# Optimization experiments

Measured on AMD Instinct MI355X. Metric: run time of the kernel, lower is better.

The kernel has to match this reference:

```python
import jax, jax.numpy as jnp
import numpy as np

B, H, W, C = 2, 384, 384, 64
WIN = 8
HEADS = 2
HD = C // HEADS
SCALE = HD ** -0.5
HID = 256  # mlp_ratio * dim
N = WIN * WIN


def _rel_index():
    # Swin-style relative position index, computed once with numpy (static).
    coords = np.stack(np.meshgrid(np.arange(WIN), np.arange(WIN), indexing='ij'))  # 2,w,w
    cf = coords.reshape(2, -1)
    rel = cf[:, :, None] - cf[:, None, :]            # 2,N,N
    rel = rel.transpose(1, 2, 0).astype(np.int64)    # N,N,2
    rel[..., 0] += WIN - 1
    rel[..., 1] += WIN - 1
    rel[..., 0] *= 2 * WIN - 1
    return jnp.asarray(rel.sum(-1))                  # N,N

REL_IDX = _rel_index()


def _ln(x, g, b):
    m = x.mean(-1, keepdims=True)
    v = ((x - m) ** 2).mean(-1, keepdims=True)
    return (x - m) * jax.lax.rsqrt(v + 1e-5) * g + b


def setup_inputs() -> dict:
    key = jax.random.key(0)
    ks = jax.random.split(key, 10)
    def n(k, shape, s=0.02):
        return jax.random.normal(k, shape, jnp.float32) * s
    return {
        'x': jax.random.normal(ks[0], (B, H * W, C), jnp.float32),
        'norm1_g': jnp.ones((C,), jnp.float32), 'norm1_b': jnp.zeros((C,), jnp.float32),
        'wq': n(ks[1], (C, C)), 'bq': jnp.zeros((C,), jnp.float32),
        'wkv': n(ks[2], (C, 2 * C)), 'bkv': jnp.zeros((2 * C,), jnp.float32),
        'rel_bias': n(ks[3], ((2 * WIN - 1) ** 2, HEADS)),
        'wproj': n(ks[4], (C, C)), 'bproj': jnp.zeros((C,), jnp.float32),
        'norm2_g': jnp.ones((C,), jnp.float32), 'norm2_b': jnp.zeros((C,), jnp.float32),
        'w1': n(ks[5], (C, HID)), 'b1': jnp.zeros((HID,), jnp.float32),
        'dwk': n(ks[6], (HID, 1, 3, 3)), 'dwb': jnp.zeros((HID,), jnp.float32),
        'w2': n(ks[7], (HID, C)), 'b2': jnp.zeros((C,), jnp.float32),
    }


def _forward(x, norm1_g, norm1_b, wq, bq, wkv, bkv, rel_bias, wproj, bproj,
             norm2_g, norm2_b, w1, b1, dwk, dwb, w2, b2):
    # --- windowed self-attention (shift_size=0, no mask) ---
    xs = _ln(x, norm1_g, norm1_b).reshape(B, H, W, C)
    win = xs.reshape(B, H // WIN, WIN, W // WIN, WIN, C)
    win = win.transpose(0, 1, 3, 2, 4, 5).reshape(-1, N, C)     # (B*nW, N, C)
    q = (win @ wq + bq).reshape(-1, N, HEADS, HD).transpose(0, 2, 1, 3)
    kv = (win @ wkv + bkv).reshape(-1, N, 2, HEADS, HD)
    k = kv[:, :, 0].transpose(0, 2, 1, 3)
    v = kv[:, :, 1].transpose(0, 2, 1, 3)
    bias = rel_bias[REL_IDX].transpose(2, 0, 1)                 # (nH, N, N)
    attn = jnp.einsum('bhnd,bhmd->bhnm', q * SCALE, k) + bias[None]
    attn = jax.nn.softmax(attn, axis=-1)
    o = jnp.einsum('bhnm,bhmd->bhnd', attn, v)
    o = o.transpose(0, 2, 1, 3).reshape(-1, N, C) @ wproj + bproj
    # window reverse
    o = o.reshape(B, H // WIN, W // WIN, WIN, WIN, C)
    o = o.transpose(0, 1, 3, 2, 4, 5).reshape(B, H * W, C)
    x = x + o
    # --- LeFF: linear -> gelu -> depthwise 3x3 -> gelu -> linear ---
    y = _ln(x, norm2_g, norm2_b)
    h = jax.nn.gelu(y @ w1 + b1, approximate=False)
    hi = h.reshape(B, H, W, HID).transpose(0, 3, 1, 2)          # NCHW
    hi = jax.lax.conv_general_dilated(
        hi, dwk, window_strides=(1, 1), padding='SAME',
        feature_group_count=HID,
        dimension_numbers=('NCHW', 'OIHW', 'NCHW')) + dwb[None, :, None, None]
    h = jax.nn.gelu(hi, approximate=False).transpose(0, 2, 3, 1).reshape(B, H * W, HID)
    return x + (h @ w2 + b2)


def reference(x, norm1_g, norm1_b, wq, bq, wkv, bkv, rel_bias, wproj, bproj,
              norm2_g, norm2_b, w1, b1, dwk, dwb, w2, b2):
    return _forward(x, norm1_g, norm1_b, wq, bq, wkv, bkv, rel_bias, wproj, bproj,
                    norm2_g, norm2_b, w1, b1, dwk, dwb, w2, b2)
```

## Files before the change

### kernel.cpp

```cpp
#include <hip/hip_runtime.h>
#include <math.h>

typedef unsigned short u16;
typedef unsigned int u32;
typedef __attribute__((ext_vector_type(8))) unsigned short us8;
typedef __attribute__((ext_vector_type(8))) __bf16 bf16x8;
typedef __attribute__((ext_vector_type(4))) float f32x4;

#define MFMA16(a, b, c) __builtin_amdgcn_mfma_f32_16x16x32_bf16((a), (b), (c), 0, 0, 0)

static __device__ __forceinline__ float bf2f(u16 u) {
  union { u32 i; float f; } v; v.i = ((u32)u) << 16; return v.f;
}
static __device__ __forceinline__ u16 f2bf(float f) {
  __bf16 h = (__bf16)f;
  return __builtin_bit_cast(u16, h);
}
static __device__ __forceinline__ u32 pk2bf(float lo, float hi) {
  return ((u32)f2bf(hi) << 16) | (u32)f2bf(lo);
}
static __device__ __forceinline__ float lo16(u32 v) {
  union { u32 i; float f; } u; u.i = v << 16; return u.f;
}
static __device__ __forceinline__ float hi16(u32 v) {
  union { u32 i; float f; } u; u.i = v & 0xFFFF0000u; return u.f;
}
static __device__ __forceinline__ bf16x8 ldfrag(const u16* p) {
  us8 v = *reinterpret_cast<const us8*>(p);
  return __builtin_bit_cast(bf16x8, v);
}
static __device__ __forceinline__ float gelu_s(float x) {
  return x * __builtin_amdgcn_rcpf(1.0f + __builtin_amdgcn_exp2f(-2.45564427f * x));
}

#define NTOK 147456
#define NWX 48

__global__ __launch_bounds__(256) void k_prep(
    const float* __restrict__ wq, const float* __restrict__ wkv,
    const float* __restrict__ wproj, const float* __restrict__ w1,
    const float* __restrict__ w2, const float* __restrict__ relb,
    u16* __restrict__ wqkvT, u16* __restrict__ wpT,
    u16* __restrict__ w1T, u16* __restrict__ w2T, float* __restrict__ biasx)
{
  const int idx = blockIdx.x * 256 + threadIdx.x;
  const int NT = 64 * 256;
  for (int i = idx; i < 12288; i += NT) {
    int o = i >> 6, c = i & 63;
    wqkvT[i] = f2bf(o < 64 ? wq[c * 64 + o] : wkv[c * 128 + (o - 64)]);
  }
  for (int i = idx; i < 4096; i += NT) {
    int o = i >> 6, c = i & 63;
    wpT[i] = f2bf(wproj[c * 64 + o]);
  }
  for (int i = idx; i < 16384; i += NT) {
    int o = i >> 6, c = i & 63;
    w1T[i] = f2bf(w1[c * 256 + o]);
  }
  for (int i = idx; i < 16384; i += NT) {
    int o = i >> 8, c2 = i & 255;
    w2T[i] = f2bf(w2[c2 * 64 + o]);
  }
  for (int i = idx; i < 8192; i += NT) {
    int h = i >> 12, r = i & 4095, ii = r >> 6, j = r & 63;
    int dy = (ii >> 3) - (j >> 3) + 7, dx = (ii & 7) - (j & 7) + 7;
    biasx[i] = relb[(dy * 15 + dx) * 2 + h];
  }
}

static __device__ __forceinline__ void softmax_rows(
    const f32x4* sc, const float* biasrow_base, int i0, int lg, int lr,
    u16* Pd)
{
#pragma unroll
  for (int r = 0; r < 4; ++r) {
    const int i = i0 + lg * 4 + r;
    const float* brow = biasrow_base + i * 64;
    float pv[4];
    float mx = -1e30f;
#pragma unroll
    for (int jt = 0; jt < 4; ++jt) {
      pv[jt] = fmaf(sc[jt][r], 0.17677669529663687f, brow[jt * 16 + lr]);
      mx = fmaxf(mx, pv[jt]);
    }
#pragma unroll
    for (int off = 1; off < 16; off <<= 1) mx = fmaxf(mx, __shfl_xor(mx, off));
    float sum = 0.f;
#pragma unroll
    for (int jt = 0; jt < 4; ++jt) { pv[jt] = __expf(pv[jt] - mx); sum += pv[jt]; }
#pragma unroll
    for (int off = 1; off < 16; off <<= 1) sum += __shfl_xor(sum, off);
    const float inv = __builtin_amdgcn_rcpf(sum);
#pragma unroll
    for (int jt = 0; jt < 4; ++jt)
      Pd[i * 72 + jt * 16 + lr] = f2bf(pv[jt] * inv);
  }
}

__global__ __launch_bounds__(256, 4) void k_attn(
    const float* __restrict__ x,
    const float* __restrict__ n1g, const float* __restrict__ n1b,
    const u16* __restrict__ wqkvT, const float* __restrict__ bq,
    const float* __restrict__ bkv, const float* __restrict__ biasx,
    const u16* __restrict__ wpT, const float* __restrict__ bproj,
    float2* __restrict__ mrs, float* __restrict__ x1)
{
  __shared__ u16 xs[64 * 72];
  __shared__ u16 qsm[64 * 72];
  __shared__ u16 ksm[64 * 72];
  __shared__ u16 vT[64 * 72];

  const int tid = threadIdx.x;
  const int wv = tid >> 6;
  const int ln = tid & 63;
  const int lg = ln >> 4, lr = ln & 15;

  const int blk = blockIdx.x;
  const int b = blk / 2304;
  const int rem = blk - b * 2304;
  const int wy = rem / NWX, wx = rem - wy * NWX;

  {
    const int t = tid >> 2, g = tid & 3;
    const int gy = wy * 8 + (t >> 3), gx = wx * 8 + (t & 7);
    const long rowbase = ((long)b * NTOK + gy * 384 + gx) * 64;
    float loc[16];
    float s0 = 0.f, s1 = 0.f;
#pragma unroll
    for (int k = 0; k < 16; k += 4) {
      float4 v4 = *reinterpret_cast<const float4*>(x + rowbase + g * 16 + k);
      loc[k] = v4.x; loc[k + 1] = v4.y; loc[k + 2] = v4.z; loc[k + 3] = v4.w;
    }
#pragma unroll
    for (int k = 0; k < 16; ++k) { s0 += loc[k]; s1 += loc[k] * loc[k]; }
    s0 += __shfl_xor(s0, 1); s0 += __shfl_xor(s0, 2);
    s1 += __shfl_xor(s1, 1); s1 += __shfl_xor(s1, 2);
    const float m = s0 * 0.015625f;
    const float var = s1 * 0.015625f - m * m;
    const float rs = rsqrtf(var + 1e-5f);
#pragma unroll
    for (int k = 0; k < 16; ++k) {
      int c = g * 16 + k;
      xs[t * 72 + c] = f2bf((loc[k] - m) * rs * n1g[c] + n1b[c]);
    }
  }
  __syncthreads();

#pragma unroll
  for (int qq = 0; qq < 3; ++qq) {
    const int grp = 3 * wv + qq;
    const int n0 = grp * 16;
    const int oc = n0 + lr;
    const float bias = (grp < 4) ? bq[oc] : bkv[oc - 64];
    bf16x8 b0 = ldfrag(&wqkvT[oc * 64 + lg * 8]);
    bf16x8 b1 = ldfrag(&wqkvT[oc * 64 + 32 + lg * 8]);
#pragma unroll
    for (int ii = 0; ii < 4; ++ii) {
      const int i0 = ii * 16;
      f32x4 acc = { bias, bias, bias, bias };
      acc = MFMA16(ldfrag(&xs[(i0 + lr) * 72 + lg * 8]), b0, acc);
      acc = MFMA16(ldfrag(&xs[(i0 + lr) * 72 + 32 + lg * 8]), b1, acc);
      const int tok0 = i0 + lg * 4;
      if (grp < 4) {
#pragma unroll
        for (int r = 0; r < 4; ++r) qsm[(tok0 + r) * 72 + oc] = f2bf(acc[r]);
      } else if (grp < 8) {
#pragma unroll
        for (int r = 0; r < 4; ++r) ksm[(tok0 + r) * 72 + (oc - 64)] = f2bf(acc[r]);
      } else {
        u32* dst = reinterpret_cast<u32*>(&vT[(oc - 128) * 72 + tok0]);
        dst[0] = pk2bf(acc[0], acc[1]);
        dst[1] = pk2bf(acc[2], acc[3]);
      }
    }
  }
  __syncthreads();

  const int i0 = wv * 16;
  f32x4 oacc[2][2];
  {
    bf16x8 aq0 = ldfrag(&qsm[(i0 + lr) * 72 + lg * 8]);
    bf16x8 aq1 = ldfrag(&qsm[(i0 + lr) * 72 + 32 + lg * 8]);
    f32x4 sc0[4], sc1[4];
#pragma unroll
    for (int jt = 0; jt < 4; ++jt) {
      f32x4 z = {};
      bf16x8 bk0 = ldfrag(&ksm[(jt * 16 + lr) * 72 + lg * 8]);
      bf16x8 bk1 = ldfrag(&ksm[(jt * 16 + lr) * 72 + 32 + lg * 8]);
      sc0[jt] = MFMA16(aq0, bk0, z);
      sc1[jt] = MFMA16(aq1, bk1, z);
    }
    softmax_rows(sc0, biasx, i0, lg, lr, xs);
    softmax_rows(sc1, biasx + 4096, i0, lg, lr, qsm);

#pragma unroll
    for (int q = 0; q < 2; ++q) {
      f32x4 a0 = {}, a1 = {};
#pragma unroll
      for (int ks = 0; ks < 64; ks += 32) {
        a0 = MFMA16(ldfrag(&xs[(i0 + lr) * 72 + ks + lg * 8]),
                    ldfrag(&vT[(q * 16 + lr) * 72 + ks + lg * 8]), a0);
        a1 = MFMA16(ldfrag(&qsm[(i0 + lr) * 72 + ks + lg * 8]),
                    ldfrag(&vT[(32 + q * 16 + lr) * 72 + ks + lg * 8]), a1);
      }
      oacc[0][q] = a0;
      oacc[1][q] = a1;
    }
  }
  __syncthreads();

#pragma unroll
  for (int h = 0; h < 2; ++h)
#pragma unroll
    for (int q = 0; q < 2; ++q) {
      const int ch = h * 32 + q * 16 + lr;
#pragma unroll
      for (int r = 0; r < 4; ++r)
        ksm[(i0 + lg * 4 + r) * 72 + ch] = f2bf(oacc[h][q][r]);
    }

  {
    float s[4] = {}, sq[4] = {};
#pragma unroll
    for (int q = 0; q < 4; ++q) {
      const int o0 = q * 16;
      const int oc = o0 + lr;
      const float bp = bproj[oc];
      f32x4 acc = { bp, bp, bp, bp };
#pragma unroll
      for (int ks = 0; ks < 64; ks += 32) {
        bf16x8 ao = ldfrag(&ksm[(i0 + lr) * 72 + ks + lg * 8]);
        bf16x8 bw = ldfrag(&wpT[(o0 + lr) * 64 + ks + lg * 8]);
        acc = MFMA16(ao, bw, acc);
      }
#pragma unroll
      for (int r = 0; r < 4; ++r) {
        const int tok = i0 + lg * 4 + r;
        const int gy = wy * 8 + (tok >> 3), gx = wx * 8 + (tok & 7);
        const long idx = ((long)b * NTOK + gy * 384 + gx) * 64 + oc;
        const float v = x[idx] + acc[r];
        x1[idx] = v;
        s[r] += v; sq[r] += v * v;
      }
    }
#pragma unroll
    for (int r = 0; r < 4; ++r) {
      float ss = s[r], qq = sq[r];
#pragma unroll
      for (int off = 1; off < 16; off <<= 1) {
        ss += __shfl_xor(ss, off);
        qq += __shfl_xor(qq, off);
      }
      if (lr == 0) {
        const float m = ss * 0.015625f;
        const float var = qq * 0.015625f - m * m;
        const int tok = i0 + lg * 4 + r;
        const int gy = wy * 8 + (tok >> 3), gx = wx * 8 + (tok & 7);
        mrs[(long)b * NTOK + gy * 384 + gx] = make_float2(m, rsqrtf(var + 1e-5f));
      }
    }
  }
}

__global__ __launch_bounds__(512, 8) void k_mlp(
    const float* __restrict__ x1, const float2* __restrict__ mrs,
    const float* __restrict__ n2g, const float* __restrict__ n2b,
    const u16* __restrict__ w1T, const float* __restrict__ pb1,
    const float* __restrict__ dwk, const float* __restrict__ dwb,
    const u16* __restrict__ w2T, const float* __restrict__ pb2,
    float* __restrict__ out)
{
  __shared__ u16 xln[112 * 72];
  __shared__ u16 htbT[64 * 102];
  __shared__ u16 g2[64 * 72];
  __shared__ float flag[112];

  const int tid = threadIdx.x;
  const int wave = tid >> 6, ln = tid & 63;
  const int lg = ln >> 4, lr = ln & 15;
  const int blk = blockIdx.x;
  const int b = blk / 2304;
  const int rem = blk - b * 2304;
  const int ty0 = (rem / NWX) * 8, tx0 = (rem - (rem / NWX) * NWX) * 8;

  if (tid < 112) {
    float f = 0.f;
    if (tid < 100) {
      const int py = ty0 + tid / 10 - 1, px = tx0 + tid % 10 - 1;
      if (py >= 0 && py < 384 && px >= 0 && px < 384) f = 1.f;
    }
    flag[tid] = f;
  }

  {
    const float gg = n2g[ln], bb = n2b[ln];
#pragma unroll
    for (int j = 0; j < 14; ++j) {
      const int p = j * 8 + wave;
      u16 o = 0;
      if (p < 100) {
        const int py = ty0 + p / 10 - 1, px = tx0 + p % 10 - 1;
        if (py >= 0 && py < 384 && px >= 0 && px < 384) {
          const long tok = (long)b * NTOK + py * 384 + px;
          const float2 mr = mrs[tok];
          const float v = x1[tok * 64 + ln];
          o = f2bf((v - mr.x) * mr.y * gg + bb);
        }
      }
      xln[p * 72 + ln] = o;
    }
  }
  __syncthreads();

  const int n0f = (wave & 3) * 16;
  const int i0b = (wave >> 2) * 16;
  const int ocf = n0f + lr;
  const int o0  = (wave >> 1) * 16;
  const int i0q = ((wave * 2) & 3) * 16;
  const int oc2 = o0 + lr;
  const float fc2_b = pb2[oc2];
  f32x4 facc[2] = { { fc2_b, fc2_b, fc2_b, fc2_b }, { fc2_b, fc2_b, fc2_b, fc2_b } };

#pragma unroll 1
  for (int ch = 0; ch < 4; ++ch) {
    {
      const u16* wbase = &w1T[(ch * 64 + ocf) * 64 + lg * 8];
      bf16x8 wb0 = ldfrag(wbase);
      bf16x8 wb1 = ldfrag(wbase + 32);
      const float bias1 = pb1[ch * 64 + ocf];
#pragma unroll
      for (int k = 0; k < 4; ++k) {
        const int i0 = i0b + k * 32;
        if (i0 < 112) {
          f32x4 acc = { bias1, bias1, bias1, bias1 };
          acc = MFMA16(ldfrag(&xln[(i0 + lr) * 72 + lg * 8]), wb0, acc);
          acc = MFMA16(ldfrag(&xln[(i0 + lr) * 72 + 32 + lg * 8]), wb1, acc);
          const int p0 = i0 + lg * 4;
          if (p0 < 100) {
            float g0 = gelu_s(acc[0]) * flag[p0 + 0];
            float g1 = gelu_s(acc[1]) * flag[p0 + 1];
            float g2v = gelu_s(acc[2]) * flag[p0 + 2];
            float g3 = gelu_s(acc[3]) * flag[p0 + 3];
            u32* dst = reinterpret_cast<u32*>(&htbT[ocf * 102 + p0]);
            dst[0] = pk2bf(g0, g1);
            dst[1] = pk2bf(g2v, g3);
          }
        }
      }
    }
    __syncthreads();

    {
      const int gch = ch * 64 + ln;
      float wk[9];
      const float db = dwb[gch];
#pragma unroll
      for (int q = 0; q < 9; ++q) wk[q] = dwk[gch * 9 + q];
      const u16* rowbase = &htbT[ln * 102];
      const u32* r0 = reinterpret_cast<const u32*>(rowbase + (wave + 0) * 10);
      const u32* r1 = reinterpret_cast<const u32*>(rowbase + (wave + 1) * 10);
      const u32* r2 = reinterpret_cast<const u32*>(rowbase + (wave + 2) * 10);
      u32 v;
      float a0,b0,c0,d0, a1,b1,c1,d1, a2,b2,c2,d2;
      v = r0[0]; a0 = lo16(v); b0 = hi16(v);
      v = r0[1]; c0 = lo16(v); d0 = hi16(v);
      v = r1[0]; a1 = lo16(v); b1 = hi16(v);
      v = r1[1]; c1 = lo16(v); d1 = hi16(v);
      v = r2[0]; a2 = lo16(v); b2 = hi16(v);
      v = r2[1]; c2 = lo16(v); d2 = hi16(v);
#pragma unroll
      for (int s = 0; s < 4; ++s) {
        float e0 = db + a0 * wk[0] + b0 * wk[1] + c0 * wk[2]
                      + a1 * wk[3] + b1 * wk[4] + c1 * wk[5]
                      + a2 * wk[6] + b2 * wk[7] + c2 * wk[8];
        float e1 = db + b0 * wk[0] + c0 * wk[1] + d0 * wk[2]
                      + b1 * wk[3] + c1 * wk[4] + d1 * wk[5]
                      + b2 * wk[6] + c2 * wk[7] + d2 * wk[8];
        g2[(wave * 8 + 2 * s) * 72 + ln]     = f2bf(gelu_s(e0));
        g2[(wave * 8 + 2 * s + 1) * 72 + ln] = f2bf(gelu_s(e1));
        if (s < 3) {
          v = r0[s + 2]; a0 = c0; b0 = d0; c0 = lo16(v); d0 = hi16(v);
          v = r1[s + 2]; a1 = c1; b1 = d1; c1 = lo16(v); d1 = hi16(v);
          v = r2[s + 2]; a2 = c2; b2 = d2; c2 = lo16(v); d2 = hi16(v);
        }
      }
    }
    __syncthreads();

    {
      const u16* wbase2 = &w2T[oc2 * 256 + ch * 64 + lg * 8];
      bf16x8 bw0 = ldfrag(wbase2);
      bf16x8 bw1 = ldfrag(wbase2 + 32);
#pragma unroll
      for (int q = 0; q < 2; ++q) {
        const int i0 = i0q + q * 16;
        bf16x8 ag0 = ldfrag(&g2[(i0 + lr) * 72 + lg * 8]);
        bf16x8 ag1 = ldfrag(&g2[(i0 + lr) * 72 + 32 + lg * 8]);
        facc[q] = MFMA16(ag0, bw0, facc[q]);
        facc[q] = MFMA16(ag1, bw1, facc[q]);
      }
    }
  }

#pragma unroll
  for (int q = 0; q < 2; ++q) {
    const int i0 = i0q + q * 16;
#pragma unroll
    for (int r = 0; r < 4; ++r) {
      const int token = i0 + lg * 4 + r;
      const int gy = ty0 + (token >> 3), gx = tx0 + (token & 7);
      const long idx = ((long)b * NTOK + gy * 384 + gx) * 64 + oc2;
      out[idx] = x1[idx] + facc[q][r];
    }
  }
}

extern "C" void kernel_launch(void* const* d_in, const int* in_sizes, int n_in,
                              void* d_out, int out_size, void* d_ws, size_t ws_size,
                              hipStream_t stream) {
  const float* x     = (const float*)d_in[0];
  const float* n1g   = (const float*)d_in[1];
  const float* n1b   = (const float*)d_in[2];
  const float* wq    = (const float*)d_in[3];
  const float* bq    = (const float*)d_in[4];
  const float* wkv   = (const float*)d_in[5];
  const float* bkv   = (const float*)d_in[6];
  const float* relb  = (const float*)d_in[7];
  const float* wproj = (const float*)d_in[8];
  const float* bproj = (const float*)d_in[9];
  const float* n2g   = (const float*)d_in[10];
  const float* n2b   = (const float*)d_in[11];
  const float* w1    = (const float*)d_in[12];
  const float* b1    = (const float*)d_in[13];
  const float* dwk   = (const float*)d_in[14];
  const float* dwb   = (const float*)d_in[15];
  const float* w2    = (const float*)d_in[16];
  const float* b2    = (const float*)d_in[17];

  char* ws = (char*)d_ws;
  u16*    wqkvT = (u16*)ws;
  u16*    wpT   = (u16*)(ws + 24576);
  u16*    w1T   = (u16*)(ws + 32768);
  u16*    w2T   = (u16*)(ws + 65536);
  float*  biasx = (float*)(ws + 98304);
  float2* mrs   = (float2*)(ws + 131072);
  float*  x1    = (float*)(ws + 2490368);
  float*  outp  = (float*)d_out;

  k_prep<<<64, 256, 0, stream>>>(wq, wkv, wproj, w1, w2, relb, wqkvT, wpT, w1T, w2T, biasx);
  k_attn<<<4608, 256, 0, stream>>>(x, n1g, n1b, wqkvT, bq, bkv, biasx, wpT, bproj, mrs, x1);
  k_mlp<<<4608, 512, 0, stream>>>(x1, mrs, n2g, n2b, w1T, b1, dwk, dwb, w2T, b2, outp);
}
```

Baseline: 221.8 us.

## Store residual and LayerNorm2 output as bf16 intermediates from attention kernel

```diff
diff --git a/kernel.cpp b/kernel.cpp
--- a/kernel.cpp
+++ b/kernel.cpp
@@ -103,7 +103,8 @@
     const u16* __restrict__ wqkvT, const float* __restrict__ bq,
     const float* __restrict__ bkv, const float* __restrict__ biasx,
     const u16* __restrict__ wpT, const float* __restrict__ bproj,
-    float2* __restrict__ mrs, float* __restrict__ x1)
+    const float* __restrict__ n2g, const float* __restrict__ n2b,
+    u16* __restrict__ x1b, u16* __restrict__ xn)
 {
   __shared__ u16 xs[64 * 72];
   __shared__ u16 qsm[64 * 72];
@@ -220,29 +221,36 @@
     }
 
   {
+    const int tok0 = i0 + lg * 4;
+    const int gy0 = wy * 8 + (tok0 >> 3), gx0 = wx * 8 + (tok0 & 7);
+    const long xbase = ((long)b * NTOK + gy0 * 384 + gx0) * 64;
+
+    float vst[4][4];
     float s[4] = {}, sq[4] = {};
 #pragma unroll
     for (int q = 0; q < 4; ++q) {
-      const int o0 = q * 16;
-      const int oc = o0 + lr;
+      const int oc = q * 16 + lr;
       const float bp = bproj[oc];
       f32x4 acc = { bp, bp, bp, bp };
 #pragma unroll
       for (int ks = 0; ks < 64; ks += 32) {
         bf16x8 ao = ldfrag(&ksm[(i0 + lr) * 72 + ks + lg * 8]);
-        bf16x8 bw = ldfrag(&wpT[(o0 + lr) * 64 + ks + lg * 8]);
+        bf16x8 bw = ldfrag(&wpT[oc * 64 + ks + lg * 8]);
         acc = MFMA16(ao, bw, acc);
       }
+      long idx = xbase + oc;
 #pragma unroll
       for (int r = 0; r < 4; ++r) {
-        const int tok = i0 + lg * 4 + r;
-        const int gy = wy * 8 + (tok >> 3), gx = wx * 8 + (tok & 7);
-        const long idx = ((long)b * NTOK + gy * 384 + gx) * 64 + oc;
         const float v = x[idx] + acc[r];
-        x1[idx] = v;
+        x1b[idx] = f2bf(v);
+        vst[q][r] = v;
         s[r] += v; sq[r] += v * v;
-      }
-    }
+        idx += 64;
+      }
+    }
+    float ng[4], nb[4];
+#pragma unroll
+    for (int q = 0; q < 4; ++q) { ng[q] = n2g[q * 16 + lr]; nb[q] = n2b[q * 16 + lr]; }
 #pragma unroll
     for (int r = 0; r < 4; ++r) {
       float ss = s[r], qq = sq[r];
@@ -251,20 +259,18 @@
         ss += __shfl_xor(ss, off);
         qq += __shfl_xor(qq, off);
       }
-      if (lr == 0) {
-        const float m = ss * 0.015625f;
-        const float var = qq * 0.015625f - m * m;
-        const int tok = i0 + lg * 4 + r;
-        const int gy = wy * 8 + (tok >> 3), gx = wx * 8 + (tok & 7);
-        mrs[(long)b * NTOK + gy * 384 + gx] = make_float2(m, rsqrtf(var + 1e-5f));
-      }
+      const float m = ss * 0.015625f;
+      const float rs = rsqrtf(qq * 0.015625f - m * m + 1e-5f);
+      const long idxn = xbase + r * 64 + lr;
+#pragma unroll
+      for (int q = 0; q < 4; ++q)
+        xn[idxn + q * 16] = f2bf((vst[q][r] - m) * rs * ng[q] + nb[q]);
     }
   }
 }
 
 __global__ __launch_bounds__(512, 8) void k_mlp(
-    const float* __restrict__ x1, const float2* __restrict__ mrs,
-    const float* __restrict__ n2g, const float* __restrict__ n2b,
+    const u16* __restrict__ x1b, const u16* __restrict__ xn,
     const u16* __restrict__ w1T, const float* __restrict__ pb1,
     const float* __restrict__ dwk, const float* __restrict__ dwb,
     const u16* __restrict__ w2T, const float* __restrict__ pb2,
@@ -293,21 +299,21 @@
   }
 
   {
-    const float gg = n2g[ln], bb = n2b[ln];
-#pragma unroll
-    for (int j = 0; j < 14; ++j) {
-      const int p = j * 8 + wave;
-      u16 o = 0;
+    const int hh = ln >> 5, c2 = ln & 31;
+    const long hbase = (long)b * NTOK + (ty0 - 1) * 384 + (tx0 - 1);
+#pragma unroll
+    for (int j = 0; j < 7; ++j) {
+      const int p = j * 16 + wave * 2 + hh;
+      u32 v = 0;
       if (p < 100) {
-        const int py = ty0 + p / 10 - 1, px = tx0 + p % 10 - 1;
-        if (py >= 0 && py < 384 && px >= 0 && px < 384) {
-          const long tok = (long)b * NTOK + py * 384 + px;
-          const float2 mr = mrs[tok];
-          const float v = x1[tok * 64 + ln];
-          o = f2bf((v - mr.x) * mr.y * gg + bb);
+        const int ry = p / 10, rx = p - ry * 10;
+        const int py = ty0 - 1 + ry, px = tx0 - 1 + rx;
+        if ((unsigned)py < 384u && (unsigned)px < 384u) {
+          const long tok = hbase + ry * 384 + rx;
+          v = *reinterpret_cast<const u32*>(&xn[tok * 64 + c2 * 2]);
         }
       }
-      xln[p * 72 + ln] = o;
+      *reinterpret_cast<u32*>(&xln[p * 72 + c2 * 2]) = v;
     }
   }
   __syncthreads();
@@ -404,13 +410,13 @@
 
 #pragma unroll
   for (int q = 0; q < 2; ++q) {
-    const int i0 = i0q + q * 16;
+    const int tok0 = i0q + q * 16 + lg * 4;
+    const int gy = ty0 + (tok0 >> 3), gx = tx0 + (tok0 & 7);
+    long idx = ((long)b * NTOK + gy * 384 + gx) * 64 + oc2;
 #pragma unroll
     for (int r = 0; r < 4; ++r) {
-      const int token = i0 + lg * 4 + r;
-      const int gy = ty0 + (token >> 3), gx = tx0 + (token & 7);
-      const long idx = ((long)b * NTOK + gy * 384 + gx) * 64 + oc2;
-      out[idx] = x1[idx] + facc[q][r];
+      out[idx] = bf2f(x1b[idx]) + facc[q][r];
+      idx += 64;
     }
   }
 }
@@ -443,11 +449,12 @@
   u16*    w1T   = (u16*)(ws + 32768);
   u16*    w2T   = (u16*)(ws + 65536);
   float*  biasx = (float*)(ws + 98304);
-  float2* mrs   = (float2*)(ws + 131072);
-  float*  x1    = (float*)(ws + 2490368);
+  u16*    x1b   = (u16*)(ws + 131072);
+  u16*    xn    = (u16*)(ws + 37879808);
   float*  outp  = (float*)d_out;
 
   k_prep<<<64, 256, 0, stream>>>(wq, wkv, wproj, w1, w2, relb, wqkvT, wpT, w1T, w2T, biasx);
-  k_attn<<<4608, 256, 0, stream>>>(x, n1g, n1b, wqkvT, bq, bkv, biasx, wpT, bproj, mrs, x1);
-  k_mlp<<<4608, 512, 0, stream>>>(x1, mrs, n2g, n2b, w1T, b1, dwk, dwb, w2T, b2, outp);
-}
+  k_attn<<<4608, 256, 0, stream>>>(x, n1g, n1b, wqkvT, bq, bkv, biasx, wpT, bproj,
+                                   n2g, n2b, x1b, xn);
+  k_mlp<<<4608, 512, 0, stream>>>(x1b, xn, w1T, b1, dwk, dwb, w2T, b2, outp);
+}
```

Measured after the change: 197.1 us. -11.1%, faster.
